# Performance work log

Hardware: AMD Instinct MI355X
Metric: run time of the kernel (lower is better)

Reference implementation:

```python
import jax, jax.numpy as jnp
import numpy as np
import math

H, W = 32, 32
HID = 256
K = 4
B = 16
DIN = 272
DFF = 1024
L = 2
NB = 7
IMG_H, IMG_W = 256, 256
LN_EPS = 1e-5


def _layernorm(x, g, b):
    m = jnp.mean(x, axis=-1, keepdims=True)
    v = jnp.var(x, axis=-1, keepdims=True)
    return (x - m) / jnp.sqrt(v + LN_EPS) * g + b


def _neighbor_mask(h, w, nb):
    # (h*w, h*w): 0 inside the nb x nb window around each query pixel, -inf outside
    rr = jnp.repeat(jnp.arange(h), w)
    cc = jnp.tile(jnp.arange(w), h)
    near = (jnp.abs(rr[:, None] - rr[None, :]) <= nb // 2) & (
        jnp.abs(cc[:, None] - cc[None, :]) <= nb // 2
    )
    return jnp.where(near, 0.0, -jnp.inf).astype(jnp.float32)


def _pos_embed(row_embed, col_embed):
    # pos[i*w + j] = concat(col_embed[j], row_embed[i])  -> (h*w, hid)
    h, nf = row_embed.shape
    w = col_embed.shape[0]
    pe = jnp.concatenate(
        [
            jnp.broadcast_to(col_embed[None, :, :], (h, w, nf)),
            jnp.broadcast_to(row_embed[:, None, :], (h, w, nf)),
        ],
        axis=-1,
    )
    return pe.reshape(h * w, 2 * nf)


def _resize_bilinear_ac(x, oh, ow):
    # nn.UpsamplingBilinear2d => align_corners=True
    b, c, h, w = x.shape
    ys = jnp.arange(oh) * ((h - 1) / (oh - 1))
    y0 = jnp.floor(ys).astype(jnp.int32)
    y1 = jnp.minimum(y0 + 1, h - 1)
    fy = (ys - y0).astype(x.dtype)
    x = x[:, :, y0, :] * (1 - fy)[None, None, :, None] + x[:, :, y1, :] * fy[None, None, :, None]
    xs = jnp.arange(ow) * ((w - 1) / (ow - 1))
    x0 = jnp.floor(xs).astype(jnp.int32)
    x1 = jnp.minimum(x0 + 1, w - 1)
    fx = (xs - x0).astype(x.dtype)
    x = x[:, :, :, x0] * (1 - fx) + x[:, :, :, x1] * fx
    return x


def _forward(query_features, matched_features, qW, qb, kvW, kvb, row_embed, col_embed,
             aggW, aggb, n1g, n1b, l1W, l1b, l2W, l2b, n2g, n2b, outW, outb):
    b, c_in, h, w = query_features.shape
    n = h * w
    # b c h w -> b (h w) c, then input projections
    qt = query_features.transpose(0, 2, 3, 1).reshape(b, n, c_in) @ qW + qb  # (b,n,hid)
    kt = matched_features.transpose(0, 1, 3, 4, 2).reshape(K, b, n, c_in) @ kvW + kvb  # (K,b,n,hid)

    pos = _pos_embed(row_embed, col_embed)  # (n, hid); broadcast over batch
    mask = _neighbor_mask(h, w, NB)  # (n, n)
    scale = 1.0 / math.sqrt(qt.shape[-1])

    x = qt
    for l in range(L):
        qp = (x + pos) * scale            # q gets pos embed then scaled
        kp = kt + pos                     # k gets pos embed; v is the raw matched tokens
        scores = jnp.einsum('bnc,kbmc->kbnm', qp, kp) + mask
        attn = jax.nn.softmax(scores, axis=-1)
        o = jnp.einsum('kbnm,kbmc->bnkc', attn, kt).reshape(b, n, K * HID)
        o = o @ aggW[l] + aggb[l]
        x = _layernorm(x + o, n1g[l], n1b[l])
        ff = jax.nn.relu(x @ l1W[l] + l1b[l]) @ l2W[l] + l2b[l]
        x = _layernorm(x + ff, n2g[l], n2b[l])

    recon_tokens = x @ outW + outb  # (b,n,c_in)
    recon = recon_tokens.reshape(b, h, w, c_in).transpose(0, 3, 1, 2)
    pred = jnp.sqrt(jnp.sum((recon - query_features) ** 2, axis=1, keepdims=True))
    pred = (pred - pred.min()) / (pred.max() - pred.min())
    pred = _resize_bilinear_ac(pred, IMG_H, IMG_W)
    return recon, pred


def setup_inputs() -> dict:
    key = jax.random.key(0)
    ks = jax.random.split(key, 12)

    def nrm(k, shape, scale=0.02):
        return jax.random.normal(k, shape, jnp.float32) * scale

    return {
        'query_features': jax.random.normal(ks[0], (B, DIN, H, W), jnp.float32),
        'matched_features': jax.random.normal(ks[1], (K, B, DIN, H, W), jnp.float32),
        'qW': nrm(ks[2], (DIN, HID)), 'qb': jnp.zeros((HID,), jnp.float32),
        'kvW': nrm(ks[3], (DIN, HID)), 'kvb': jnp.zeros((HID,), jnp.float32),
        'row_embed': jax.random.uniform(ks[4], (H, HID // 2), jnp.float32),
        'col_embed': jax.random.uniform(ks[5], (W, HID // 2), jnp.float32),
        'aggW': nrm(ks[6], (L, K * HID, HID)), 'aggb': jnp.zeros((L, HID), jnp.float32),
        'n1g': jnp.ones((L, HID), jnp.float32), 'n1b': jnp.zeros((L, HID), jnp.float32),
        'l1W': nrm(ks[7], (L, HID, DFF)), 'l1b': jnp.zeros((L, DFF), jnp.float32),
        'l2W': nrm(ks[8], (L, DFF, HID)), 'l2b': jnp.zeros((L, HID), jnp.float32),
        'n2g': jnp.ones((L, HID), jnp.float32), 'n2b': jnp.zeros((L, HID), jnp.float32),
        'outW': nrm(ks[9], (HID, DIN)), 'outb': jnp.zeros((DIN,), jnp.float32),
    }


def reference(query_features, matched_features, qW, qb, kvW, kvb, row_embed, col_embed,
              aggW, aggb, n1g, n1b, l1W, l1b, l2W, l2b, n2g, n2b, outW, outb):
    return _forward(query_features, matched_features, qW, qb, kvW, kvb, row_embed,
                    col_embed, aggW, aggb, n1g, n1b, l1W, l1b, l2W, l2b, n2g, n2b,
                    outW, outb)
```

## Files before the change

kernel.cpp:

```cpp
#include <hip/hip_runtime.h>
#include <hip/hip_bf16.h>
#include <math.h>

#define BATCH 16
#define NTOK 1024
#define HID 256
#define KMEM 4
#define DIN 272
#define DINP 288
#define DFF 1024
#define LN_EPS 1e-5f

using short8 = __attribute__((ext_vector_type(8))) short;
using short4v = __attribute__((ext_vector_type(4))) short;
using floatx4 = __attribute__((ext_vector_type(4))) float;

__device__ inline short f2bf(float f) {
  unsigned u = __builtin_bit_cast(unsigned, f);
  u += 0x7fff + ((u >> 16) & 1);
  return (short)(u >> 16);
}
__device__ inline float bf2f(short s) {
  unsigned u = ((unsigned)(unsigned short)s) << 16;
  return __builtin_bit_cast(float, u);
}

__global__ __launch_bounds__(256) void pos_kernel(
    const float* __restrict__ row_e, const float* __restrict__ col_e,
    float* __restrict__ pos) {
  int t = blockIdx.x;
  int j = threadIdx.x;
  float v = (j < 128) ? col_e[(t & 31) * 128 + j]
                      : row_e[(t >> 5) * 128 + (j - 128)];
  pos[t * 256 + j] = v;
}

__global__ __launch_bounds__(256) void tcvt_kernel(
    const float* __restrict__ src, short* __restrict__ dst) {
  __shared__ short tile[32][33];
  int slice = blockIdx.x >> 5;
  int t0 = (blockIdx.x & 31) * 32;
  int c0 = blockIdx.y * 32;
  int tx = threadIdx.x & 31, ty = threadIdx.x >> 5;
  const float* s = src + (long)slice * DIN * NTOK;
#pragma unroll
  for (int i = 0; i < 4; i++) {
    int c = c0 + ty + i * 8;
    float v = (c < DIN) ? s[(long)c * NTOK + t0 + tx] : 0.f;
    tile[ty + i * 8][tx] = f2bf(v);
  }
  __syncthreads();
  short* d = dst + ((long)slice * NTOK + t0) * DINP + c0;
#pragma unroll
  for (int i = 0; i < 4; i++) {
    int tl = ty + i * 8;
    d[(long)tl * DINP + tx] = tile[tx][tl];
  }
}

struct WtJob {
  const float* src;
  short* dst;
  int K, Kd, N, ntx, start;
};
struct WtJobs {
  WtJob j[9];
};

__global__ __launch_bounds__(256) void wt_cvt_all_kernel(WtJobs jobs) {
  __shared__ short tile[32][33];
  int bid = blockIdx.x;
  int ji = 0;
#pragma unroll
  for (int i = 1; i < 9; ++i)
    if (bid >= jobs.j[i].start) ji = i;
  const float* W = jobs.j[ji].src;
  short* Wt = jobs.j[ji].dst;
  int K = jobs.j[ji].K, Kd = jobs.j[ji].Kd, N = jobs.j[ji].N;
  int local = bid - jobs.j[ji].start;
  int n0 = (local % jobs.j[ji].ntx) * 32;
  int k0 = (local / jobs.j[ji].ntx) * 32;
  int tx = threadIdx.x & 31, ty8 = threadIdx.x >> 5;
#pragma unroll
  for (int i = 0; i < 4; i++) {
    int k = k0 + ty8 + i * 8;
    int n = n0 + tx;
    float v = (k < K && n < N) ? W[(long)k * N + n] : 0.f;
    tile[ty8 + i * 8][tx] = f2bf(v);
  }
  __syncthreads();
#pragma unroll
  for (int i = 0; i < 4; i++) {
    int n = n0 + ty8 + i * 8;
    int k = k0 + tx;
    if (n < N && k < Kd) Wt[(long)n * Kd + k] = tile[tx][ty8 + i * 8];
  }
}

template <int OUTMODE>
__global__ __launch_bounds__(256) void gemm2_kernel(
    const short* __restrict__ A, const short* __restrict__ Wt,
    const float* __restrict__ bias, float* __restrict__ Cf,
    short* __restrict__ Cs, int M, int N, int K, int gxn,
    short* __restrict__ ktp, short* __restrict__ ktv,
    const float* __restrict__ pos) {
  __shared__ short As[2][64][40];
  __shared__ short Bs[2][128][40];
  int nwg = gridDim.x;
  int cpx = nwg >> 3;
  int bid = blockIdx.x;
  int h = (bid & 7) * cpx + (bid >> 3);
  int cx = h % gxn;
  int ry = h / gxn;
  int row0 = ry * 64, col0 = cx * 128;
  int tid = threadIdx.x;
  int w = tid >> 6, lane = tid & 63;
  int wrow = (w >> 1) * 32, wcol = (w & 1) * 64;
  int lcol = lane & 15, kg = lane >> 4;

  int arow = tid >> 2, ak = (tid & 3) * 8;
  int brow = tid >> 2, bk = (tid & 3) * 8;
  const short* Ab = A + (long)row0 * K;
  const short* Bb = Wt + (long)col0 * K;
  bool bv0 = (col0 + brow) < N;
  bool bv1 = (col0 + brow + 64) < N;

  const short8 z8 = (short8){0, 0, 0, 0, 0, 0, 0, 0};
  short8 ra, rb0, rb1;
  ra = *reinterpret_cast<const short8*>(&Ab[(long)arow * K + ak]);
  rb0 = bv0 ? *reinterpret_cast<const short8*>(&Bb[(long)brow * K + bk]) : z8;
  rb1 = bv1 ? *reinterpret_cast<const short8*>(&Bb[(long)(brow + 64) * K + bk])
            : z8;
  *reinterpret_cast<short8*>(&As[0][arow][ak]) = ra;
  *reinterpret_cast<short8*>(&Bs[0][brow][bk]) = rb0;
  *reinterpret_cast<short8*>(&Bs[0][brow + 64][bk]) = rb1;
  __syncthreads();

  floatx4 acc[2][4];
#pragma unroll
  for (int m = 0; m < 2; ++m)
#pragma unroll
    for (int n = 0; n < 4; ++n) acc[m][n] = (floatx4){0.f, 0.f, 0.f, 0.f};

  int NT = K >> 5;
  for (int t = 0; t < NT; ++t) {
    int cur = t & 1;
    if (t + 1 < NT) {
      int ko = (t + 1) << 5;
      ra = *reinterpret_cast<const short8*>(&Ab[(long)arow * K + ko + ak]);
      rb0 = bv0 ? *reinterpret_cast<const short8*>(&Bb[(long)brow * K + ko + bk])
                : z8;
      rb1 = bv1 ? *reinterpret_cast<const short8*>(
                      &Bb[(long)(brow + 64) * K + ko + bk])
                : z8;
    }
    short8 af[2], bf[4];
#pragma unroll
    for (int m = 0; m < 2; ++m)
      af[m] = *reinterpret_cast<const short8*>(
          &As[cur][wrow + m * 16 + lcol][kg * 8]);
#pragma unroll
    for (int n = 0; n < 4; ++n)
      bf[n] = *reinterpret_cast<const short8*>(
          &Bs[cur][wcol + n * 16 + lcol][kg * 8]);
#pragma unroll
    for (int m = 0; m < 2; ++m)
#pragma unroll
      for (int n = 0; n < 4; ++n)
        acc[m][n] = __builtin_amdgcn_mfma_f32_16x16x32_bf16(af[m], bf[n],
                                                            acc[m][n], 0, 0, 0);
    if (t + 1 < NT) {
      int nxt = cur ^ 1;
      *reinterpret_cast<short8*>(&As[nxt][arow][ak]) = ra;
      *reinterpret_cast<short8*>(&Bs[nxt][brow][bk]) = rb0;
      *reinterpret_cast<short8*>(&Bs[nxt][brow + 64][bk]) = rb1;
    }
    __syncthreads();
  }

#pragma unroll
  for (int n = 0; n < 4; ++n) {
    int c = col0 + wcol + n * 16 + lcol;
    if (c >= N) continue;
    float bv = bias[c];
#pragma unroll
    for (int m = 0; m < 2; ++m) {
      int rbase = row0 + wrow + m * 16 + kg * 4;
      if (OUTMODE == 0) {
#pragma unroll
        for (int q = 0; q < 4; ++q)
          Cf[(long)(rbase + q) * N + c] = acc[m][n][q] + bv;
      } else if (OUTMODE == 1) {
#pragma unroll
        for (int q = 0; q < 4; ++q)
          Cs[(long)(rbase + q) * N + c] = f2bf(fmaxf(acc[m][n][q] + bv, 0.f));
      } else if (OUTMODE == 3) {
#pragma unroll
        for (int q = 0; q < 4; ++q) {
          float val = acc[m][n][q] + bv;
          Cf[(long)(rbase + q) * N + c] = val;
          Cs[(long)(rbase + q) * N + c] = f2bf(val);
        }
      } else {
        int slice = rbase >> 10, tbase = rbase & 1023;
        short4v vt;
#pragma unroll
        for (int q = 0; q < 4; ++q) {
          float val = acc[m][n][q] + bv;
          vt[q] = f2bf(val);
          ktp[(long)(rbase + q) * 256 + c] =
              f2bf(val + pos[(tbase + q) * 256 + c]);
        }
        *reinterpret_cast<short4v*>(
            &ktv[(long)slice * (256 * 1024) + (long)c * 1024 + tbase]) = vt;
      }
    }
  }
}

__global__ __launch_bounds__(256) void gemm_ln_kernel(
    const short* __restrict__ A, const short* __restrict__ Wt,
    const float* __restrict__ bias, const float* __restrict__ res,
    const float* __restrict__ g, const float* __restrict__ bta,
    float* __restrict__ xout, short* __restrict__ x16out, int K) {
  __shared__ short As[2][32][40];
  __shared__ short Bs[2][256][40];
  __shared__ float st_s[32][4];
  __shared__ float st_s2[32][4];
  int tid = threadIdx.x;
  int row0 = blockIdx.x * 32;
  int w = tid >> 6, lane = tid & 63, lcol = lane & 15, kg = lane >> 4;
  int arow = tid >> 2, ak = (tid & 3) * 8;
  int brow = tid >> 2, bk = (tid & 3) * 8;
  const short* Ab = A + (long)row0 * K;

  short8 ra, rb[4];
  if (tid < 128) ra = *reinterpret_cast<const short8*>(&Ab[(long)arow * K + ak]);
#pragma unroll
  for (int i = 0; i < 4; ++i)
    rb[i] = *reinterpret_cast<const short8*>(&Wt[(long)(brow + i * 64) * K + bk]);
  if (tid < 128) *reinterpret_cast<short8*>(&As[0][arow][ak]) = ra;
#pragma unroll
  for (int i = 0; i < 4; ++i)
    *reinterpret_cast<short8*>(&Bs[0][brow + i * 64][bk]) = rb[i];
  __syncthreads();

  floatx4 acc[2][4];
#pragma unroll
  for (int m = 0; m < 2; ++m)
#pragma unroll
    for (int n = 0; n < 4; ++n) acc[m][n] = (floatx4){0.f, 0.f, 0.f, 0.f};

  int NT = K >> 5;
  for (int t = 0; t < NT; ++t) {
    int cur = t & 1;
    if (t + 1 < NT) {
      int ko = (t + 1) << 5;
      if (tid < 128)
        ra = *reinterpret_cast<const short8*>(&Ab[(long)arow * K + ko + ak]);
#pragma unroll
      for (int i = 0; i < 4; ++i)
        rb[i] = *reinterpret_cast<const short8*>(
            &Wt[(long)(brow + i * 64) * K + ko + bk]);
    }
    short8 af[2], bf[4];
#pragma unroll
    for (int m = 0; m < 2; ++m)
      af[m] =
          *reinterpret_cast<const short8*>(&As[cur][m * 16 + lcol][kg * 8]);
#pragma unroll
    for (int n = 0; n < 4; ++n)
      bf[n] = *reinterpret_cast<const short8*>(
          &Bs[cur][w * 64 + n * 16 + lcol][kg * 8]);
#pragma unroll
    for (int m = 0; m < 2; ++m)
#pragma unroll
      for (int n = 0; n < 4; ++n)
        acc[m][n] = __builtin_amdgcn_mfma_f32_16x16x32_bf16(af[m], bf[n],
                                                            acc[m][n], 0, 0, 0);
    if (t + 1 < NT) {
      int nxt = cur ^ 1;
      if (tid < 128) *reinterpret_cast<short8*>(&As[nxt][arow][ak]) = ra;
#pragma unroll
      for (int i = 0; i < 4; ++i)
        *reinterpret_cast<short8*>(&Bs[nxt][brow + i * 64][bk]) = rb[i];
    }
    __syncthreads();
  }

  float val[2][4][4];
#pragma unroll
  for (int n = 0; n < 4; ++n) {
    int c = w * 64 + n * 16 + lcol;
    float bv = bias[c];
#pragma unroll
    for (int m = 0; m < 2; ++m) {
      int rbase = row0 + m * 16 + kg * 4;
#pragma unroll
      for (int q = 0; q < 4; ++q)
        val[m][n][q] = acc[m][n][q] + bv + res[(long)(rbase + q) * 256 + c];
    }
  }
  float s[2][4], s2[2][4];
#pragma unroll
  for (int m = 0; m < 2; ++m)
#pragma unroll
    for (int q = 0; q < 4; ++q) {
      float ss = 0.f, ss2 = 0.f;
#pragma unroll
      for (int n = 0; n < 4; ++n) {
        float v = val[m][n][q];
        ss += v;
        ss2 = fmaf(v, v, ss2);
      }
      ss += __shfl_xor(ss, 1);
      ss2 += __shfl_xor(ss2, 1);
      ss += __shfl_xor(ss, 2);
      ss2 += __shfl_xor(ss2, 2);
      ss += __shfl_xor(ss, 4);
      ss2 += __shfl_xor(ss2, 4);
      ss += __shfl_xor(ss, 8);
      ss2 += __shfl_xor(ss2, 8);
      s[m][q] = ss;
      s2[m][q] = ss2;
    }
  if (lcol == 0) {
#pragma unroll
    for (int m = 0; m < 2; ++m)
#pragma unroll
      for (int q = 0; q < 4; ++q) {
        st_s[m * 16 + kg * 4 + q][w] = s[m][q];
        st_s2[m * 16 + kg * 4 + q][w] = s2[m][q];
      }
  }
  __syncthreads();
#pragma unroll
  for (int m = 0; m < 2; ++m)
#pragma unroll
    for (int q = 0; q < 4; ++q) {
      int row = m * 16 + kg * 4 + q;
      float4 a4 = *reinterpret_cast<const float4*>(&st_s[row][0]);
      float4 b4 = *reinterpret_cast<const float4*>(&st_s2[row][0]);
      float S = (a4.x + a4.y) + (a4.z + a4.w);
      float S2 = (b4.x + b4.y) + (b4.z + b4.w);
      float mean = S * (1.f / 256.f);
      float var = S2 * (1.f / 256.f) - mean * mean;
      float inv = rsqrtf(var + LN_EPS);
#pragma unroll
      for (int n = 0; n < 4; ++n) {
        int c = w * 64 + n * 16 + lcol;
        float o = (val[m][n][q] - mean) * inv * g[c] + bta[c];
        long addr = (long)(row0 + row) * 256 + c;
        xout[addr] = o;
        x16out[addr] = f2bf(o);
      }
    }
}

__global__ __launch_bounds__(256) void attn_kernel(
    const short* __restrict__ x16, const short* __restrict__ ktp,
    const short* __restrict__ ktv, const float* __restrict__ pos,
    short* __restrict__ o) {
  __shared__ short Q_s[32][264];
  __shared__ short P_s[32][264];
  __shared__ float st_mx[32][4];
  __shared__ float st_sm[32][4];
  int h = blockIdx.x;
  int xcd = h & 7, jj = h >> 3;
  int sidx = xcd * 8 + (jj >> 5);
  int r = jj & 31;
  int b = sidx & 15, k = sidx >> 4;
  int tid = threadIdx.x;
  int w = tid >> 6, lane = tid & 63, lcol = lane & 15, kg = lane >> 4;
  const float scale = 0.0625f;

  const short* xb = x16 + ((long)b * NTOK + r * 32) * HID;
  const float* pq = pos + (long)r * 32 * HID;
#pragma unroll
  for (int p = 0; p < 4; ++p) {
    int f = p * 256 + tid;
    int row = f >> 5, c8 = (f & 31) << 3;
    short8 xv = *reinterpret_cast<const short8*>(&xb[row * HID + c8]);
    float4 p0 = *reinterpret_cast<const float4*>(&pq[row * HID + c8]);
    float4 p1 = *reinterpret_cast<const float4*>(&pq[row * HID + c8 + 4]);
    short8 s;
    s[0] = f2bf((bf2f(xv[0]) + p0.x) * scale);
    s[1] = f2bf((bf2f(xv[1]) + p0.y) * scale);
    s[2] = f2bf((bf2f(xv[2]) + p0.z) * scale);
    s[3] = f2bf((bf2f(xv[3]) + p0.w) * scale);
    s[4] = f2bf((bf2f(xv[4]) + p1.x) * scale);
    s[5] = f2bf((bf2f(xv[5]) + p1.y) * scale);
    s[6] = f2bf((bf2f(xv[6]) + p1.z) * scale);
    s[7] = f2bf((bf2f(xv[7]) + p1.w) * scale);
    *reinterpret_cast<short8*>(&Q_s[row][c8]) = s;
  }
  __syncthreads();

  int r0 = max(r - 3, 0), r1 = min(r + 3, 31);
  int nkr = r1 - r0 + 1, nm = nkr * 32;
  const short* ktpb = ktp + ((long)(k * BATCH + b)) * NTOK * HID;
  const short* ktvb = ktv + ((long)(k * BATCH + b)) * NTOK * HID;

  floatx4 acc[2][4];
#pragma unroll
  for (int m = 0; m < 2; ++m)
#pragma unroll
    for (int n = 0; n < 4; ++n) acc[m][n] = (floatx4){0.f, 0.f, 0.f, 0.f};

  int tokn[4];
#pragma unroll
  for (int n = 0; n < 4; ++n) {
    int nf = w * 4 + n;
    int krow = min(r0 + (nf >> 1), 31);
    tokn[n] = krow * 32 + ((nf & 1) << 4) + lcol;
  }
#pragma unroll
  for (int s = 0; s < 8; ++s) {
    short8 af0 = *reinterpret_cast<const short8*>(&Q_s[lcol][s * 32 + kg * 8]);
    short8 af1 =
        *reinterpret_cast<const short8*>(&Q_s[16 + lcol][s * 32 + kg * 8]);
#pragma unroll
    for (int n = 0; n < 4; ++n) {
      short8 bfr = *reinterpret_cast<const short8*>(
          &ktpb[(long)tokn[n] * HID + s * 32 + kg * 8]);
      acc[0][n] =
          __builtin_amdgcn_mfma_f32_16x16x32_bf16(af0, bfr, acc[0][n], 0, 0, 0);
      acc[1][n] =
          __builtin_amdgcn_mfma_f32_16x16x32_bf16(af1, bfr, acc[1][n], 0, 0, 0);
    }
  }

  const float NEG = -3.0e38f;
  float mx[2][4];
#pragma unroll
  for (int m = 0; m < 2; ++m)
#pragma unroll
    for (int q = 0; q < 4; ++q) {
      int rr = m * 16 + kg * 4 + q;
      float vmax = NEG;
#pragma unroll
      for (int n = 0; n < 4; ++n) {
        int col = (w * 4 + n) * 16 + lcol;
        int ck = col & 31;
        bool ok = (col < nm) && (ck - rr <= 3) && (rr - ck <= 3);
        float v = ok ? acc[m][n][q] : NEG;
        acc[m][n][q] = v;
        vmax = fmaxf(vmax, v);
      }
      vmax = fmaxf(vmax, __shfl_xor(vmax, 1));
      vmax = fmaxf(vmax, __shfl_xor(vmax, 2));
      vmax = fmaxf(vmax, __shfl_xor(vmax, 4));
      vmax = fmaxf(vmax, __shfl_xor(vmax, 8));
      mx[m][q] = vmax;
    }
  if (lcol == 0) {
#pragma unroll
    for (int m = 0; m < 2; ++m)
#pragma unroll
      for (int q = 0; q < 4; ++q) st_mx[m * 16 + kg * 4 + q][w] = mx[m][q];
  }
  __syncthreads();
  float sm[2][4];
#pragma unroll
  for (int m = 0; m < 2; ++m)
#pragma unroll
    for (int q = 0; q < 4; ++q) {
      int rr = m * 16 + kg * 4 + q;
      float4 v4 = *reinterpret_cast<const float4*>(&st_mx[rr][0]);
      float g = fmaxf(fmaxf(v4.x, v4.y), fmaxf(v4.z, v4.w));
      float ss = 0.f;
#pragma unroll
      for (int n = 0; n < 4; ++n) {
        float v = acc[m][n][q];
        float pv = (v > -1.0e30f) ? exp2f((v - g) * 1.4426950408889634f) : 0.f;
        acc[m][n][q] = pv;
        ss += pv;
      }
      ss += __shfl_xor(ss, 1);
      ss += __shfl_xor(ss, 2);
      ss += __shfl_xor(ss, 4);
      ss += __shfl_xor(ss, 8);
      sm[m][q] = ss;
    }
  if (lcol == 0) {
#pragma unroll
    for (int m = 0; m < 2; ++m)
#pragma unroll
      for (int q = 0; q < 4; ++q) st_sm[m * 16 + kg * 4 + q][w] = sm[m][q];
  }
  __syncthreads();
#pragma unroll
  for (int m = 0; m < 2; ++m)
#pragma unroll
    for (int q = 0; q < 4; ++q) {
      int rr = m * 16 + kg * 4 + q;
      float4 v4 = *reinterpret_cast<const float4*>(&st_sm[rr][0]);
      float rinv = 1.0f / (v4.x + v4.y + v4.z + v4.w);
#pragma unroll
      for (int n = 0; n < 4; ++n) {
        P_s[rr][(w * 4 + n) * 16 + lcol] = f2bf(acc[m][n][q] * rinv);
      }
    }
  __syncthreads();

  floatx4 oacc[2][4];
#pragma unroll
  for (int m = 0; m < 2; ++m)
#pragma unroll
    for (int n = 0; n < 4; ++n) oacc[m][n] = (floatx4){0.f, 0.f, 0.f, 0.f};

  for (int kb = 0; kb < nkr; ++kb) {
    short8 ap0 = *reinterpret_cast<const short8*>(&P_s[lcol][kb * 32 + kg * 8]);
    short8 ap1 =
        *reinterpret_cast<const short8*>(&P_s[16 + lcol][kb * 32 + kg * 8]);
    int tokb = (r0 + kb) * 32;
#pragma unroll
    for (int n = 0; n < 4; ++n) {
      int ch = w * 64 + n * 16 + lcol;
      short8 bv = *reinterpret_cast<const short8*>(
          &ktvb[(long)ch * NTOK + tokb + kg * 8]);
      oacc[0][n] =
          __builtin_amdgcn_mfma_f32_16x16x32_bf16(ap0, bv, oacc[0][n], 0, 0, 0);
      oacc[1][n] =
          __builtin_amdgcn_mfma_f32_16x16x32_bf16(ap1, bv, oacc[1][n], 0, 0, 0);
    }
  }
#pragma unroll
  for (int m = 0; m < 2; ++m)
#pragma unroll
    for (int n = 0; n < 4; ++n) {
      int ch = w * 64 + n * 16 + lcol;
#pragma unroll
      for (int q = 0; q < 4; ++q) {
        int rr = m * 16 + kg * 4 + q;
        o[((long)b * NTOK + r * 32 + rr) * (KMEM * HID) + k * HID + ch] =
            f2bf(oacc[m][n][q]);
      }
    }
}

__global__ __launch_bounds__(256) void recon_out_kernel(
    const float* __restrict__ rt, const float* __restrict__ qf,
    float* __restrict__ recon, float* __restrict__ pred_sq) {
  int b = blockIdx.y;
  int t0 = blockIdx.x * 32;
  __shared__ float tile[32][33];
  int lx = threadIdx.x & 31;
  int ly = threadIdx.x >> 5;
  float sq = 0.f;
  for (int c0 = 0; c0 < DIN; c0 += 32) {
    __syncthreads();
#pragma unroll
    for (int i = 0; i < 4; i++) {
      int tt = ly + i * 8;
      int c = c0 + lx;
      tile[tt][lx] = (c < DIN) ? rt[((long)b * NTOK + t0 + tt) * DIN + c] : 0.f;
    }
    __syncthreads();
#pragma unroll
    for (int i = 0; i < 4; i++) {
      int c = c0 + ly + i * 8;
      if (c < DIN) {
        float v = tile[lx][ly + i * 8];
        long gaddr = ((long)b * DIN + c) * NTOK + t0 + lx;
        float q = qf[gaddr];
        recon[gaddr] = v;
        float d = v - q;
        sq = fmaf(d, d, sq);
      }
    }
  }
  __shared__ float red[8][33];
  red[ly][lx] = sq;
  __syncthreads();
  if (ly == 0) {
    float s = 0.f;
#pragma unroll
    for (int u = 0; u < 8; u++) s += red[u][lx];
    pred_sq[b * NTOK + t0 + lx] = s;
  }
}

__global__ __launch_bounds__(256) void minmax_kernel(
    const float* __restrict__ pred_sq, float* __restrict__ mnmx) {
  int tid = threadIdx.x;
  float mn = INFINITY, mx = -INFINITY;
  for (int i = tid; i < BATCH * NTOK; i += 256) {
    float v = sqrtf(pred_sq[i]);
    mn = fminf(mn, v);
    mx = fmaxf(mx, v);
  }
#pragma unroll
  for (int off = 32; off > 0; off >>= 1) {
    mn = fminf(mn, __shfl_xor(mn, off));
    mx = fmaxf(mx, __shfl_xor(mx, off));
  }
  __shared__ float smn[4], smx[4];
  int wave = tid >> 6, lane = tid & 63;
  if (lane == 0) {
    smn[wave] = mn;
    smx[wave] = mx;
  }
  __syncthreads();
  if (tid == 0) {
    mn = fminf(fminf(smn[0], smn[1]), fminf(smn[2], smn[3]));
    mx = fmaxf(fmaxf(smx[0], smx[1]), fmaxf(smx[2], smx[3]));
    mnmx[0] = mn;
    mnmx[1] = mx;
  }
}

__global__ __launch_bounds__(256) void resize_kernel(
    const float* __restrict__ pred_sq, const float* __restrict__ mnmx,
    float* __restrict__ out) {
  long idx = (long)blockIdx.x * 256 + threadIdx.x;
  if (idx >= (long)BATCH * 256 * 256) return;
  int b = (int)(idx >> 16);
  int oy = (int)((idx >> 8) & 255), ox = (int)(idx & 255);
  float mn = mnmx[0], mx = mnmx[1];
  float inv = 1.0f / (mx - mn);
  float ys = oy * (31.0f / 255.0f);
  int y0 = (int)floorf(ys);
  int y1 = min(y0 + 1, 31);
  float fy = ys - (float)y0;
  float xs = ox * (31.0f / 255.0f);
  int x0 = (int)floorf(xs);
  int x1 = min(x0 + 1, 31);
  float fx = xs - (float)x0;
  const float* p = pred_sq + b * NTOK;
  float v00 = sqrtf(p[y0 * 32 + x0]), v01 = sqrtf(p[y0 * 32 + x1]);
  float v10 = sqrtf(p[y1 * 32 + x0]), v11 = sqrtf(p[y1 * 32 + x1]);
  float cA = v00 * (1.f - fy) + v10 * fy;
  float cB = v01 * (1.f - fy) + v11 * fy;
  float v = cA * (1.f - fx) + cB * fx;
  out[idx] = (v - mn) * inv;
}

extern "C" void kernel_launch(void* const* d_in, const int* in_sizes, int n_in,
                              void* d_out, int out_size, void* d_ws,
                              size_t ws_size, hipStream_t stream) {
  const float* qf = (const float*)d_in[0];
  const float* mf = (const float*)d_in[1];
  const float* qW = (const float*)d_in[2];
  const float* qb = (const float*)d_in[3];
  const float* kvW = (const float*)d_in[4];
  const float* kvb = (const float*)d_in[5];
  const float* row_e = (const float*)d_in[6];
  const float* col_e = (const float*)d_in[7];
  const float* aggW = (const float*)d_in[8];
  const float* aggb = (const float*)d_in[9];
  const float* n1g = (const float*)d_in[10];
  const float* n1b = (const float*)d_in[11];
  const float* l1W = (const float*)d_in[12];
  const float* l1b = (const float*)d_in[13];
  const float* l2W = (const float*)d_in[14];
  const float* l2b = (const float*)d_in[15];
  const float* n2g = (const float*)d_in[16];
  const float* n2b = (const float*)d_in[17];
  const float* outW = (const float*)d_in[18];
  const float* outb = (const float*)d_in[19];

  float* out = (float*)d_out;
  float* recon = out;
  float* pred = out + (long)BATCH * DIN * NTOK;

  short* wt = (short*)d_out;
  short* wt_agg0 = wt;
  short* wt_agg1 = wt_agg0 + 262144;
  short* wt_l1_0 = wt_agg1 + 262144;
  short* wt_l1_1 = wt_l1_0 + 262144;
  short* wt_l2_0 = wt_l1_1 + 262144;
  short* wt_l2_1 = wt_l2_0 + 262144;
  short* wt_out = wt_l2_1 + 262144;
  short* wt_q = wt_out + 69632;
  short* wt_kv = wt_q + 73728;

  float* ws = (float*)d_ws;
  float* pos = ws;
  float* x = pos + 262144;
  short* x16 = (short*)(x + 4194304);
  short* ktp = x16 + 4194304;
  short* ktv = ktp + 16777216;
  short* buf16 = ktv + 16777216;
  float* tmp256 = (float*)(buf16 + 16777216);
  float* rtbuf = tmp256 + 4194304;
  float* pred_sq = rtbuf + 4456448;
  float* mnmx = pred_sq + 16384;
  short* qf_t = ktp;
  short* mf_t = buf16;

  pos_kernel<<<NTOK, 256, 0, stream>>>(row_e, col_e, pos);

  {
    WtJobs jobs;
    jobs.j[0] = {aggW, wt_agg0, 1024, 1024, 256, 8, 0};
    jobs.j[1] = {aggW + 262144, wt_agg1, 1024, 1024, 256, 8, 256};
    jobs.j[2] = {l1W, wt_l1_0, 256, 256, 1024, 32, 512};
    jobs.j[3] = {l1W + 262144, wt_l1_1, 256, 256, 1024, 32, 768};
    jobs.j[4] = {l2W, wt_l2_0, 1024, 1024, 256, 8, 1024};
    jobs.j[5] = {l2W + 262144, wt_l2_1, 1024, 1024, 256, 8, 1280};
    jobs.j[6] = {outW, wt_out, 256, 256, 272, 9, 1536};
    jobs.j[7] = {qW, wt_q, 272, 288, 256, 8, 1608};
    jobs.j[8] = {kvW, wt_kv, 272, 288, 256, 8, 1680};
    wt_cvt_all_kernel<<<1752, 256, 0, stream>>>(jobs);
  }

  tcvt_kernel<<<dim3(512, 9), 256, 0, stream>>>(qf, qf_t);
  gemm2_kernel<3><<<512, 256, 0, stream>>>(qf_t, wt_q, qb, x, x16,
                                           BATCH * NTOK, HID, DINP, 2, nullptr,
                                           nullptr, nullptr);
  tcvt_kernel<<<dim3(2048, 9), 256, 0, stream>>>(mf, mf_t);
  gemm2_kernel<2><<<2048, 256, 0, stream>>>(mf_t, wt_kv, kvb, nullptr, nullptr,
                                            KMEM * BATCH * NTOK, HID, DINP, 2,
                                            ktp, ktv, pos);

  for (int l = 0; l < 2; l++) {
    attn_kernel<<<2048, 256, 0, stream>>>(x16, ktp, ktv, pos, buf16);
    gemm_ln_kernel<<<512, 256, 0, stream>>>(
        buf16, l ? wt_agg1 : wt_agg0, aggb + l * 256, x, n1g + l * 256,
        n1b + l * 256, x, x16, KMEM * HID);
    gemm2_kernel<1><<<2048, 256, 0, stream>>>(
        x16, l ? wt_l1_1 : wt_l1_0, l1b + l * 1024, nullptr, buf16,
        BATCH * NTOK, DFF, HID, 8, nullptr, nullptr, nullptr);
    gemm_ln_kernel<<<512, 256, 0, stream>>>(
        buf16, l ? wt_l2_1 : wt_l2_0, l2b + l * 256, x, n2g + l * 256,
        n2b + l * 256, x, x16, DFF);
  }

  gemm2_kernel<0><<<768, 256, 0, stream>>>(x16, wt_out, outb, rtbuf, nullptr,
                                           BATCH * NTOK, DIN, HID, 3, nullptr,
                                           nullptr, nullptr);
  {
    dim3 grid(NTOK / 32, BATCH);
    recon_out_kernel<<<grid, 256, 0, stream>>>(rtbuf, qf, recon, pred_sq);
  }
  minmax_kernel<<<1, 256, 0, stream>>>(pred_sq, mnmx);
  resize_kernel<<<(BATCH * 256 * 256) / 256, 256, 0, stream>>>(pred_sq, mnmx,
                                                               pred);
}
```

Measured before the change: 444.3 us.

## Fuse output projection with recon transpose and squared-error reduction; merge tcvt launches

The output GEMM now writes the reconstruction directly in channel-major layout and computes per-token squared-error partial sums against the query features. This removes the intermediate rtbuf and the separate recon_out transpose kernel. The minmax kernel sums the three column-tile partials. The two transpose-convert launches are merged into one grid, and the attention kernel reuses a single shared buffer for Q and P. Weight buffers move from the output area into the workspace so recon can be written in place.

```diff
diff --git a/kernel.cpp b/kernel.cpp
--- a/kernel.cpp
+++ b/kernel.cpp
@@ -36,13 +36,22 @@
 }
 
 __global__ __launch_bounds__(256) void tcvt_kernel(
-    const float* __restrict__ src, short* __restrict__ dst) {
+    const float* __restrict__ qf, const float* __restrict__ mf,
+    short* __restrict__ qf_t, short* __restrict__ mf_t) {
   __shared__ short tile[32][33];
   int slice = blockIdx.x >> 5;
   int t0 = (blockIdx.x & 31) * 32;
   int c0 = blockIdx.y * 32;
   int tx = threadIdx.x & 31, ty = threadIdx.x >> 5;
-  const float* s = src + (long)slice * DIN * NTOK;
+  const float* s;
+  short* d;
+  if (slice < 16) {
+    s = qf + (long)slice * DIN * NTOK;
+    d = qf_t + (long)slice * NTOK * DINP;
+  } else {
+    s = mf + (long)(slice - 16) * DIN * NTOK;
+    d = mf_t + (long)(slice - 16) * NTOK * DINP;
+  }
 #pragma unroll
   for (int i = 0; i < 4; i++) {
     int c = c0 + ty + i * 8;
@@ -50,7 +59,7 @@
     tile[ty + i * 8][tx] = f2bf(v);
   }
   __syncthreads();
-  short* d = dst + ((long)slice * NTOK + t0) * DINP + c0;
+  d += (long)t0 * DINP + c0;
 #pragma unroll
   for (int i = 0; i < 4; i++) {
     int tl = ty + i * 8;
@@ -103,9 +112,11 @@
     const float* __restrict__ bias, float* __restrict__ Cf,
     short* __restrict__ Cs, int M, int N, int K, int gxn,
     short* __restrict__ ktp, short* __restrict__ ktv,
-    const float* __restrict__ pos) {
+    const float* __restrict__ pos, const float* __restrict__ qfp,
+    float* __restrict__ ppart) {
   __shared__ short As[2][64][40];
   __shared__ short Bs[2][128][40];
+  __shared__ float part_s[64][2];
   int nwg = gridDim.x;
   int cpx = nwg >> 3;
   int bid = blockIdx.x;
@@ -176,6 +187,55 @@
       *reinterpret_cast<short8*>(&Bs[nxt][brow + 64][bk]) = rb1;
     }
     __syncthreads();
+  }
+
+  if (OUTMODE == 4) {
+    int bb = row0 >> 10;
+    int tb0 = (row0 & 1023) + wrow;
+    float sqp[2][4] = {};
+#pragma unroll
+    for (int n = 0; n < 4; ++n) {
+      int c = col0 + wcol + n * 16 + lcol;
+      if (c < N) {
+        float bv = bias[c];
+#pragma unroll
+        for (int m = 0; m < 2; ++m) {
+          int tb = tb0 + m * 16 + kg * 4;
+          long addr = ((long)bb * DIN + c) * 1024 + tb;
+          float4 qv = *reinterpret_cast<const float4*>(&qfp[addr]);
+          float4 ov;
+          float v0 = acc[m][n][0] + bv;
+          float v1 = acc[m][n][1] + bv;
+          float v2 = acc[m][n][2] + bv;
+          float v3 = acc[m][n][3] + bv;
+          ov.x = v0;
+          ov.y = v1;
+          ov.z = v2;
+          ov.w = v3;
+          float d0 = v0 - qv.x, d1 = v1 - qv.y, d2 = v2 - qv.z, d3 = v3 - qv.w;
+          sqp[m][0] = fmaf(d0, d0, sqp[m][0]);
+          sqp[m][1] = fmaf(d1, d1, sqp[m][1]);
+          sqp[m][2] = fmaf(d2, d2, sqp[m][2]);
+          sqp[m][3] = fmaf(d3, d3, sqp[m][3]);
+          *reinterpret_cast<float4*>(&Cf[addr]) = ov;
+        }
+      }
+    }
+#pragma unroll
+    for (int m = 0; m < 2; ++m)
+#pragma unroll
+      for (int q = 0; q < 4; ++q) {
+        float s = sqp[m][q];
+        s += __shfl_xor(s, 1);
+        s += __shfl_xor(s, 2);
+        s += __shfl_xor(s, 4);
+        s += __shfl_xor(s, 8);
+        if (lcol == 0) part_s[wrow + m * 16 + kg * 4 + q][w & 1] = s;
+      }
+    __syncthreads();
+    if (tid < 64)
+      ppart[(long)cx * 16384 + row0 + tid] = part_s[tid][0] + part_s[tid][1];
+    return;
   }
 
 #pragma unroll
@@ -361,8 +421,7 @@
     const short* __restrict__ x16, const short* __restrict__ ktp,
     const short* __restrict__ ktv, const float* __restrict__ pos,
     short* __restrict__ o) {
-  __shared__ short Q_s[32][264];
-  __shared__ short P_s[32][264];
+  __shared__ short QP_s[32][264];
   __shared__ float st_mx[32][4];
   __shared__ float st_sm[32][4];
   int h = blockIdx.x;
@@ -392,7 +451,7 @@
     s[5] = f2bf((bf2f(xv[5]) + p1.y) * scale);
     s[6] = f2bf((bf2f(xv[6]) + p1.z) * scale);
     s[7] = f2bf((bf2f(xv[7]) + p1.w) * scale);
-    *reinterpret_cast<short8*>(&Q_s[row][c8]) = s;
+    *reinterpret_cast<short8*>(&QP_s[row][c8]) = s;
   }
   __syncthreads();
 
@@ -416,9 +475,9 @@
   }
 #pragma unroll
   for (int s = 0; s < 8; ++s) {
-    short8 af0 = *reinterpret_cast<const short8*>(&Q_s[lcol][s * 32 + kg * 8]);
+    short8 af0 = *reinterpret_cast<const short8*>(&QP_s[lcol][s * 32 + kg * 8]);
     short8 af1 =
-        *reinterpret_cast<const short8*>(&Q_s[16 + lcol][s * 32 + kg * 8]);
+        *reinterpret_cast<const short8*>(&QP_s[16 + lcol][s * 32 + kg * 8]);
 #pragma unroll
     for (int n = 0; n < 4; ++n) {
       short8 bfr = *reinterpret_cast<const short8*>(
@@ -498,7 +557,7 @@
       float rinv = 1.0f / (v4.x + v4.y + v4.z + v4.w);
 #pragma unroll
       for (int n = 0; n < 4; ++n) {
-        P_s[rr][(w * 4 + n) * 16 + lcol] = f2bf(acc[m][n][q] * rinv);
+        QP_s[rr][(w * 4 + n) * 16 + lcol] = f2bf(acc[m][n][q] * rinv);
       }
     }
   __syncthreads();
@@ -510,9 +569,9 @@
     for (int n = 0; n < 4; ++n) oacc[m][n] = (floatx4){0.f, 0.f, 0.f, 0.f};
 
   for (int kb = 0; kb < nkr; ++kb) {
-    short8 ap0 = *reinterpret_cast<const short8*>(&P_s[lcol][kb * 32 + kg * 8]);
+    short8 ap0 = *reinterpret_cast<const short8*>(&QP_s[lcol][kb * 32 + kg * 8]);
     short8 ap1 =
-        *reinterpret_cast<const short8*>(&P_s[16 + lcol][kb * 32 + kg * 8]);
+        *reinterpret_cast<const short8*>(&QP_s[16 + lcol][kb * 32 + kg * 8]);
     int tokb = (r0 + kb) * 32;
 #pragma unroll
     for (int n = 0; n < 4; ++n) {
@@ -539,56 +598,17 @@
     }
 }
 
-__global__ __launch_bounds__(256) void recon_out_kernel(
-    const float* __restrict__ rt, const float* __restrict__ qf,
-    float* __restrict__ recon, float* __restrict__ pred_sq) {
-  int b = blockIdx.y;
-  int t0 = blockIdx.x * 32;
-  __shared__ float tile[32][33];
-  int lx = threadIdx.x & 31;
-  int ly = threadIdx.x >> 5;
-  float sq = 0.f;
-  for (int c0 = 0; c0 < DIN; c0 += 32) {
-    __syncthreads();
-#pragma unroll
-    for (int i = 0; i < 4; i++) {
-      int tt = ly + i * 8;
-      int c = c0 + lx;
-      tile[tt][lx] = (c < DIN) ? rt[((long)b * NTOK + t0 + tt) * DIN + c] : 0.f;
-    }
-    __syncthreads();
-#pragma unroll
-    for (int i = 0; i < 4; i++) {
-      int c = c0 + ly + i * 8;
-      if (c < DIN) {
-        float v = tile[lx][ly + i * 8];
-        long gaddr = ((long)b * DIN + c) * NTOK + t0 + lx;
-        float q = qf[gaddr];
-        recon[gaddr] = v;
-        float d = v - q;
-        sq = fmaf(d, d, sq);
-      }
-    }
-  }
-  __shared__ float red[8][33];
-  red[ly][lx] = sq;
-  __syncthreads();
-  if (ly == 0) {
-    float s = 0.f;
-#pragma unroll
-    for (int u = 0; u < 8; u++) s += red[u][lx];
-    pred_sq[b * NTOK + t0 + lx] = s;
-  }
-}
-
 __global__ __launch_bounds__(256) void minmax_kernel(
-    const float* __restrict__ pred_sq, float* __restrict__ mnmx) {
+    const float* __restrict__ ppart, float* __restrict__ pred_sq,
+    float* __restrict__ mnmx) {
   int tid = threadIdx.x;
   float mn = INFINITY, mx = -INFINITY;
   for (int i = tid; i < BATCH * NTOK; i += 256) {
-    float v = sqrtf(pred_sq[i]);
-    mn = fminf(mn, v);
-    mx = fmaxf(mx, v);
+    float v = ppart[i] + ppart[16384 + i] + ppart[32768 + i];
+    pred_sq[i] = v;
+    float sv = sqrtf(v);
+    mn = fminf(mn, sv);
+    mx = fmaxf(mx, sv);
   }
 #pragma unroll
   for (int off = 32; off > 0; off >>= 1) {
@@ -664,7 +684,15 @@
   float* recon = out;
   float* pred = out + (long)BATCH * DIN * NTOK;
 
-  short* wt = (short*)d_out;
+  float* ws = (float*)d_ws;
+  float* pos = ws;
+  float* x = pos + 262144;
+  short* x16 = (short*)(x + 4194304);
+  short* ktp = x16 + 4194304;
+  short* ktv = ktp + 16777216;
+  short* buf16 = ktv + 16777216;
+  float* tmp256 = (float*)(buf16 + 16777216);
+  short* wt = (short*)(tmp256 + 4194304);
   short* wt_agg0 = wt;
   short* wt_agg1 = wt_agg0 + 262144;
   short* wt_l1_0 = wt_agg1 + 262144;
@@ -674,17 +702,8 @@
   short* wt_out = wt_l2_1 + 262144;
   short* wt_q = wt_out + 69632;
   short* wt_kv = wt_q + 73728;
-
-  float* ws = (float*)d_ws;
-  float* pos = ws;
-  float* x = pos + 262144;
-  short* x16 = (short*)(x + 4194304);
-  short* ktp = x16 + 4194304;
-  short* ktv = ktp + 16777216;
-  short* buf16 = ktv + 16777216;
-  float* tmp256 = (float*)(buf16 + 16777216);
-  float* rtbuf = tmp256 + 4194304;
-  float* pred_sq = rtbuf + 4456448;
+  float* pred_part = (float*)(wt_kv + 73728);
+  float* pred_sq = pred_part + 49152;
   float* mnmx = pred_sq + 16384;
   short* qf_t = ktp;
   short* mf_t = buf16;
@@ -705,14 +724,14 @@
     wt_cvt_all_kernel<<<1752, 256, 0, stream>>>(jobs);
   }
 
-  tcvt_kernel<<<dim3(512, 9), 256, 0, stream>>>(qf, qf_t);
-  gemm2_kernel<3><<<512, 256, 0, stream>>>(qf_t, wt_q, qb, x, x16,
-                                           BATCH * NTOK, HID, DINP, 2, nullptr,
-                                           nullptr, nullptr);
-  tcvt_kernel<<<dim3(2048, 9), 256, 0, stream>>>(mf, mf_t);
-  gemm2_kernel<2><<<2048, 256, 0, stream>>>(mf_t, wt_kv, kvb, nullptr, nullptr,
-                                            KMEM * BATCH * NTOK, HID, DINP, 2,
-                                            ktp, ktv, pos);
+  tcvt_kernel<<<dim3(2560, 9), 256, 0, stream>>>(qf, mf, qf_t, mf_t);
+
+  gemm2_kernel<3><<<512, 256, 0, stream>>>(
+      qf_t, wt_q, qb, x, x16, BATCH * NTOK, HID, DINP, 2, nullptr, nullptr,
+      nullptr, nullptr, nullptr);
+  gemm2_kernel<2><<<2048, 256, 0, stream>>>(
+      mf_t, wt_kv, kvb, nullptr, nullptr, KMEM * BATCH * NTOK, HID, DINP, 2,
+      ktp, ktv, pos, nullptr, nullptr);
 
   for (int l = 0; l < 2; l++) {
     attn_kernel<<<2048, 256, 0, stream>>>(x16, ktp, ktv, pos, buf16);
@@ -721,20 +740,17 @@
         n1b + l * 256, x, x16, KMEM * HID);
     gemm2_kernel<1><<<2048, 256, 0, stream>>>(
         x16, l ? wt_l1_1 : wt_l1_0, l1b + l * 1024, nullptr, buf16,
-        BATCH * NTOK, DFF, HID, 8, nullptr, nullptr, nullptr);
+        BATCH * NTOK, DFF, HID, 8, nullptr, nullptr, nullptr, nullptr,
+        nullptr);
     gemm_ln_kernel<<<512, 256, 0, stream>>>(
         buf16, l ? wt_l2_1 : wt_l2_0, l2b + l * 256, x, n2g + l * 256,
         n2b + l * 256, x, x16, DFF);
   }
 
-  gemm2_kernel<0><<<768, 256, 0, stream>>>(x16, wt_out, outb, rtbuf, nullptr,
-                                           BATCH * NTOK, DIN, HID, 3, nullptr,
-                                           nullptr, nullptr);
-  {
-    dim3 grid(NTOK / 32, BATCH);
-    recon_out_kernel<<<grid, 256, 0, stream>>>(rtbuf, qf, recon, pred_sq);
-  }
-  minmax_kernel<<<1, 256, 0, stream>>>(pred_sq, mnmx);
+  gemm2_kernel<4><<<768, 256, 0, stream>>>(
+      x16, wt_out, outb, recon, nullptr, BATCH * NTOK, DIN, HID, 3, nullptr,
+      nullptr, nullptr, qf, pred_part);
+  minmax_kernel<<<1, 256, 0, stream>>>(pred_part, pred_sq, mnmx);
   resize_kernel<<<(BATCH * 256 * 256) / 256, 256, 0, stream>>>(pred_sq, mnmx,
                                                                pred);
 }
```

After: 420.7 us. 5.3% less time.
